# Performance work log

Measured on AMD Instinct MI355X. Metric: run time of the kernel, lower is better.

Reference implementation:

```python
import jax, jax.numpy as jnp
import numpy as np

TOP_K = 2


def setup_inputs() -> dict:
    key = jax.random.key(0)
    k1, k2, k3, k4, k5 = jax.random.split(key, 5)
    H, F, E = 1024, 2048, 8
    B, S = 2, 1024
    return {
        "hidden_states": jax.random.normal(k1, (B, S, H), dtype=jnp.float32),
        "gate_w": jax.random.normal(k2, (E, H), dtype=jnp.float32) * (1.0 / np.sqrt(H)),
        "w1": jax.random.normal(k3, (E, F, H), dtype=jnp.float32) * (1.0 / np.sqrt(H)),
        "w2": jax.random.normal(k4, (E, H, F), dtype=jnp.float32) * (1.0 / np.sqrt(F)),
        "w3": jax.random.normal(k5, (E, F, H), dtype=jnp.float32) * (1.0 / np.sqrt(H)),
    }


def reference(hidden_states, gate_w, w1, w2, w3):
    B, S, H = hidden_states.shape
    E = gate_w.shape[0]
    x = hidden_states.reshape(-1, H)  # [T, H]

    # Router: softmax in float32, top-k, renormalize (exact Mixtral math)
    router_logits = x @ gate_w.T  # [T, E]
    probs = jax.nn.softmax(router_logits.astype(jnp.float32), axis=-1)
    routing_weights, selected = jax.lax.top_k(probs, TOP_K)  # [T, K]
    routing_weights = routing_weights / routing_weights.sum(axis=-1, keepdims=True)
    routing_weights = routing_weights.astype(x.dtype)

    # Per-token combine weight for each expert: [T, E]
    combine = (jax.nn.one_hot(selected, E, dtype=x.dtype) * routing_weights[..., None]).sum(axis=1)

    # Dense grouped expert SwiGLU MLP (zero combine weight for unselected experts
    # makes this strictly equivalent to the gathered/dispatched computation)
    h = jnp.einsum('th,efh->etf', x, w1)   # [E, T, F]
    g = jnp.einsum('th,efh->etf', x, w3)   # [E, T, F]
    mid = jax.nn.silu(h) * g               # SwiGLU
    expert_out = jnp.einsum('etf,ehf->eth', mid, w2)  # [E, T, H]
    out = jnp.einsum('eth,te->th', expert_out, combine)  # weighted combine

    return out.reshape(B, S, H), router_logits
```

## Files before the change

### kernel.cpp

```cpp
#include <hip/hip_runtime.h>
#include <hip/hip_bf16.h>
#include <math.h>

#define H 1024
#define FF 2048
#define E 8
#define T 2048
#define NSLOT (2*T)
#define SLOT_PAD 128

typedef __attribute__((ext_vector_type(8))) short s16x8;
typedef __attribute__((ext_vector_type(4))) float f32x4;

static __device__ __forceinline__ unsigned short f2bf(float f) {
    union { float f; unsigned u; } v; v.f = f;
    unsigned r = v.u + 0x7fff + ((v.u >> 16) & 1);
    return (unsigned short)(r >> 16);
}
static __device__ __forceinline__ float bf2f(unsigned short s) {
    union { unsigned u; float f; } v; v.u = ((unsigned)s) << 16;
    return v.f;
}

typedef __attribute__((address_space(3))) unsigned int lds_uint;
typedef const __attribute__((address_space(1))) unsigned int glob_uint;
static __device__ __forceinline__ void gl_lds16(const void* g, void* l) {
    __builtin_amdgcn_global_load_lds((glob_uint*)g, (lds_uint*)l, 16, 0, 0);
}

__global__ __launch_bounds__(256) void convert_kernel(
    const float* __restrict__ w1, const float* __restrict__ w3,
    const float* __restrict__ w2, unsigned short* __restrict__ w1b,
    unsigned short* __restrict__ w3b, unsigned short* __restrict__ w2b)
{
    const float* s; unsigned short* d;
    if (blockIdx.y == 0)      { s = w1; d = w1b; }
    else if (blockIdx.y == 1) { s = w3; d = w3b; }
    else                      { s = w2; d = w2b; }
    size_t i = ((size_t)blockIdx.x * 256 + threadIdx.x) * 8;
    float4 a = *(const float4*)(s + i);
    float4 b = *(const float4*)(s + i + 4);
    uint4 st;
    st.x = f2bf(a.x) | ((unsigned)f2bf(a.y) << 16);
    st.y = f2bf(a.z) | ((unsigned)f2bf(a.w) << 16);
    st.z = f2bf(b.x) | ((unsigned)f2bf(b.y) << 16);
    st.w = f2bf(b.z) | ((unsigned)f2bf(b.w) << 16);
    *(uint4*)(d + i) = st;
}

__global__ __launch_bounds__(256) void router_kernel(
    const float* __restrict__ x, const float* __restrict__ gw,
    float* __restrict__ logits_out, int* __restrict__ top_id,
    float* __restrict__ top_w, int* __restrict__ counts)
{
    int t = blockIdx.x;
    int tid = threadIdx.x;
    int e = tid >> 5;
    int l32 = tid & 31;
    const float* xr = x + (size_t)t * H;
    const float* gr = gw + (size_t)e * H;
    float s = 0.f;
    for (int h = l32; h < H; h += 32) s += xr[h] * gr[h];
    for (int off = 16; off; off >>= 1) s += __shfl_down(s, off, 32);
    __shared__ float lg[E];
    if (l32 == 0) lg[e] = s;
    __syncthreads();
    if (tid < E) logits_out[(size_t)t * E + tid] = lg[tid];
    if (tid == 0) {
        int i1 = 0; float b1 = lg[0];
        for (int i = 1; i < E; ++i) if (lg[i] > b1) { b1 = lg[i]; i1 = i; }
        int i2 = -1; float b2 = -INFINITY;
        for (int i = 0; i < E; ++i) if (i != i1 && lg[i] > b2) { b2 = lg[i]; i2 = i; }
        float p2 = expf(b2 - b1);
        float inv = 1.f / (1.f + p2);
        top_id[2*t]   = i1;  top_id[2*t+1] = i2;
        top_w[2*t]    = inv; top_w[2*t+1]  = p2 * inv;
        atomicAdd(&counts[i1], 1);
        atomicAdd(&counts[i2], 1);
    }
}

__global__ void scan_kernel(const int* __restrict__ counts,
                            int* __restrict__ offsets, int* __restrict__ cursors)
{
    if (threadIdx.x == 0) {
        int acc = 0;
        for (int i = 0; i < E; ++i) { offsets[i] = acc; acc += counts[i]; }
        offsets[E] = acc;
    }
    if (threadIdx.x < E) cursors[threadIdx.x] = 0;
}

__global__ __launch_bounds__(256) void assign_kernel(
    const float* __restrict__ x, const int* __restrict__ top_id,
    const int* __restrict__ offsets, int* __restrict__ cursors,
    int* __restrict__ top_pos, unsigned short* __restrict__ xg)
{
    int t = blockIdx.x, tid = threadIdx.x;
    __shared__ int pos[2];
    if (tid == 0) {
        for (int k = 0; k < 2; ++k) {
            int e = top_id[2*t + k];
            int p = offsets[e] + atomicAdd(&cursors[e], 1);
            top_pos[2*t + k] = p;
            pos[k] = p;
        }
    }
    __syncthreads();
    float4 xv = ((const float4*)(x + (size_t)t * H))[tid];
    ushort4 b;
    b.x = f2bf(xv.x); b.y = f2bf(xv.y); b.z = f2bf(xv.z); b.w = f2bf(xv.w);
    ((ushort4*)(xg + (size_t)pos[0] * H))[tid] = b;
    ((ushort4*)(xg + (size_t)pos[1] * H))[tid] = b;
}

__global__ __launch_bounds__(256) void gemm1_kernel(
    const unsigned short* __restrict__ xg,
    const unsigned short* __restrict__ w1b, const unsigned short* __restrict__ w3b,
    const int* __restrict__ offsets, unsigned short* __restrict__ mid)
{
    int e = blockIdx.z;
    int off = offsets[e];
    int cnt = offsets[e + 1] - off;
    int m0 = blockIdx.y * 128;
    if (m0 >= cnt) return;
    int f0 = blockIdx.x * 64;

    __shared__ __align__(16) unsigned short sx[128 * 64];
    __shared__ __align__(16) unsigned short s1[64 * 64];
    __shared__ __align__(16) unsigned short s3[64 * 64];

    int tid = threadIdx.x;
    int wv = tid >> 6, ln = tid & 63;
    int quad = ln >> 4, l16 = ln & 15;
    int wm = wv & 1, wn = wv >> 1;
    int xor7 = l16 & 7;

    const unsigned short* xsrc[4]; unsigned short* xdst[4];
    #pragma unroll
    for (int j = 0; j < 4; ++j) {
        int row = wv * 32 + j * 8 + (ln >> 3);
        int cl = (ln & 7) ^ (row & 7);
        xsrc[j] = xg + (size_t)(off + m0 + row) * H + cl * 8;
        xdst[j] = &sx[(wv * 32 + j * 8) * 64];
    }
    const unsigned short *w1s[2], *w3s[2]; unsigned short *d1[2], *d3[2];
    #pragma unroll
    for (int j = 0; j < 2; ++j) {
        int row = wv * 16 + j * 8 + (ln >> 3);
        int cl = (ln & 7) ^ (row & 7);
        w1s[j] = w1b + ((size_t)e * FF + f0 + row) * H + cl * 8;
        w3s[j] = w3b + ((size_t)e * FF + f0 + row) * H + cl * 8;
        d1[j] = &s1[(wv * 16 + j * 8) * 64];
        d3[j] = &s3[(wv * 16 + j * 8) * 64];
    }

    f32x4 acc1[4][2], acc3[4][2];
    #pragma unroll
    for (int i = 0; i < 4; ++i)
        #pragma unroll
        for (int j = 0; j < 2; ++j) {
            acc1[i][j] = (f32x4){0.f, 0.f, 0.f, 0.f};
            acc3[i][j] = (f32x4){0.f, 0.f, 0.f, 0.f};
        }

    for (int k0 = 0; k0 < H; k0 += 64) {
        #pragma unroll
        for (int j = 0; j < 4; ++j) gl_lds16(xsrc[j] + k0, xdst[j]);
        #pragma unroll
        for (int j = 0; j < 2; ++j) { gl_lds16(w1s[j] + k0, d1[j]); gl_lds16(w3s[j] + k0, d3[j]); }
        __syncthreads();
        #pragma unroll
        for (int ks = 0; ks < 2; ++ks) {
            int cph = ((quad + 4 * ks) ^ xor7) << 3;
            s16x8 a[4], b1v[2], b3v[2];
            #pragma unroll
            for (int i = 0; i < 4; ++i)
                a[i] = *(const s16x8*)&sx[(wm * 64 + i * 16 + l16) * 64 + cph];
            #pragma unroll
            for (int j = 0; j < 2; ++j) {
                b1v[j] = *(const s16x8*)&s1[(wn * 32 + j * 16 + l16) * 64 + cph];
                b3v[j] = *(const s16x8*)&s3[(wn * 32 + j * 16 + l16) * 64 + cph];
            }
            #pragma unroll
            for (int i = 0; i < 4; ++i)
                #pragma unroll
                for (int j = 0; j < 2; ++j) {
                    acc1[i][j] = __builtin_amdgcn_mfma_f32_16x16x32_bf16(a[i], b1v[j], acc1[i][j], 0, 0, 0);
                    acc3[i][j] = __builtin_amdgcn_mfma_f32_16x16x32_bf16(a[i], b3v[j], acc3[i][j], 0, 0, 0);
                }
        }
        __syncthreads();
    }

    #pragma unroll
    for (int i = 0; i < 4; ++i) {
        #pragma unroll
        for (int r = 0; r < 4; ++r) {
            int row = wm * 64 + i * 16 + quad * 4 + r;
            if (m0 + row < cnt) {
                size_t base = (size_t)(off + m0 + row) * FF + f0 + wn * 32;
                #pragma unroll
                for (int j = 0; j < 2; ++j) {
                    float h = acc1[i][j][r];
                    float g = acc3[i][j][r];
                    float v = h / (1.f + __expf(-h)) * g;
                    mid[base + j * 16 + l16] = f2bf(v);
                }
            }
        }
    }
}

__global__ __launch_bounds__(256) void gemm2_kernel(
    const unsigned short* __restrict__ mid, const unsigned short* __restrict__ w2b,
    const int* __restrict__ offsets, unsigned short* __restrict__ y)
{
    int e = blockIdx.z;
    int off = offsets[e];
    int cnt = offsets[e + 1] - off;
    int m0 = blockIdx.y * 128;
    if (m0 >= cnt) return;
    int n0 = blockIdx.x * 64;

    __shared__ __align__(16) unsigned short sa[128 * 64];
    __shared__ __align__(16) unsigned short sb[64 * 64];

    int tid = threadIdx.x;
    int wv = tid >> 6, ln = tid & 63;
    int quad = ln >> 4, l16 = ln & 15;
    int wm = wv & 1, wn = wv >> 1;
    int xor7 = l16 & 7;

    const unsigned short* asrc[4]; unsigned short* adst[4];
    #pragma unroll
    for (int j = 0; j < 4; ++j) {
        int row = wv * 32 + j * 8 + (ln >> 3);
        int cl = (ln & 7) ^ (row & 7);
        asrc[j] = mid + (size_t)(off + m0 + row) * FF + cl * 8;
        adst[j] = &sa[(wv * 32 + j * 8) * 64];
    }
    const unsigned short* bsrc[2]; unsigned short* bdst[2];
    #pragma unroll
    for (int j = 0; j < 2; ++j) {
        int row = wv * 16 + j * 8 + (ln >> 3);
        int cl = (ln & 7) ^ (row & 7);
        bsrc[j] = w2b + ((size_t)e * H + n0 + row) * FF + cl * 8;
        bdst[j] = &sb[(wv * 16 + j * 8) * 64];
    }

    f32x4 acc[4][2];
    #pragma unroll
    for (int i = 0; i < 4; ++i)
        #pragma unroll
        for (int j = 0; j < 2; ++j) acc[i][j] = (f32x4){0.f, 0.f, 0.f, 0.f};

    for (int k0 = 0; k0 < FF; k0 += 64) {
        #pragma unroll
        for (int j = 0; j < 4; ++j) gl_lds16(asrc[j] + k0, adst[j]);
        #pragma unroll
        for (int j = 0; j < 2; ++j) gl_lds16(bsrc[j] + k0, bdst[j]);
        __syncthreads();
        #pragma unroll
        for (int ks = 0; ks < 2; ++ks) {
            int cph = ((quad + 4 * ks) ^ xor7) << 3;
            s16x8 a[4], b[2];
            #pragma unroll
            for (int i = 0; i < 4; ++i)
                a[i] = *(const s16x8*)&sa[(wm * 64 + i * 16 + l16) * 64 + cph];
            #pragma unroll
            for (int j = 0; j < 2; ++j)
                b[j] = *(const s16x8*)&sb[(wn * 32 + j * 16 + l16) * 64 + cph];
            #pragma unroll
            for (int i = 0; i < 4; ++i)
                #pragma unroll
                for (int j = 0; j < 2; ++j)
                    acc[i][j] = __builtin_amdgcn_mfma_f32_16x16x32_bf16(a[i], b[j], acc[i][j], 0, 0, 0);
        }
        __syncthreads();
    }

    #pragma unroll
    for (int i = 0; i < 4; ++i) {
        #pragma unroll
        for (int r = 0; r < 4; ++r) {
            int row = wm * 64 + i * 16 + quad * 4 + r;
            if (m0 + row < cnt) {
                size_t base = (size_t)(off + m0 + row) * H + n0 + wn * 32;
                #pragma unroll
                for (int j = 0; j < 2; ++j)
                    y[base + j * 16 + l16] = f2bf(acc[i][j][r]);
            }
        }
    }
}

__global__ __launch_bounds__(256) void combine_kernel(
    const unsigned short* __restrict__ y, const int* __restrict__ top_pos,
    const float* __restrict__ top_w, float* __restrict__ out)
{
    int t = blockIdx.x, tid = threadIdx.x;
    int p0 = top_pos[2*t], p1 = top_pos[2*t+1];
    float w0 = top_w[2*t], w1 = top_w[2*t+1];
    ushort4 a = ((const ushort4*)(y + (size_t)p0 * H))[tid];
    ushort4 b = ((const ushort4*)(y + (size_t)p1 * H))[tid];
    float4 o;
    o.x = w0 * bf2f(a.x) + w1 * bf2f(b.x);
    o.y = w0 * bf2f(a.y) + w1 * bf2f(b.y);
    o.z = w0 * bf2f(a.z) + w1 * bf2f(b.z);
    o.w = w0 * bf2f(a.w) + w1 * bf2f(b.w);
    ((float4*)(out + (size_t)t * H))[tid] = o;
}

extern "C" void kernel_launch(void* const* d_in, const int* in_sizes, int n_in,
                              void* d_out, int out_size, void* d_ws, size_t ws_size,
                              hipStream_t stream) {
    const float* x  = (const float*)d_in[0];
    const float* gw = (const float*)d_in[1];
    const float* w1 = (const float*)d_in[2];
    const float* w2 = (const float*)d_in[3];
    const float* w3 = (const float*)d_in[4];
    float* out    = (float*)d_out;
    float* logits = out + (size_t)T * H;

    int* counts   = (int*)d_ws;
    int* cursors  = counts + 8;
    int* offsets  = counts + 16;
    int* top_id   = counts + 32;
    int* top_pos  = top_id + 2*T;
    float* top_w  = (float*)(top_pos + 2*T);
    unsigned short* xg  = (unsigned short*)(top_w + 2*T);
    unsigned short* mid = xg  + (size_t)(NSLOT + SLOT_PAD) * H;
    unsigned short* y   = mid + (size_t)(NSLOT + SLOT_PAD) * FF;
    unsigned short* w1b = y   + (size_t)NSLOT * H;
    unsigned short* w3b = w1b + (size_t)E * FF * H;
    unsigned short* w2b = w3b + (size_t)E * FF * H;

    hipMemsetAsync(counts, 0, 16 * sizeof(int), stream);

    convert_kernel<<<dim3((E*FF*H)/(256*8), 3), 256, 0, stream>>>(w1, w3, w2, w1b, w3b, w2b);
    router_kernel<<<T, 256, 0, stream>>>(x, gw, logits, top_id, top_w, counts);
    scan_kernel<<<1, 64, 0, stream>>>(counts, offsets, cursors);
    assign_kernel<<<T, 256, 0, stream>>>(x, top_id, offsets, cursors, top_pos, xg);
    gemm1_kernel<<<dim3(FF / 64, 16, E), 256, 0, stream>>>(xg, w1b, w3b, offsets, mid);
    gemm2_kernel<<<dim3(H / 64, 16, E), 256, 0, stream>>>(mid, w2b, offsets, y);
    combine_kernel<<<T, 256, 0, stream>>>(y, top_pos, top_w, out);
}
```

Before: 426.3 us.

## Fuse weight conversion with router, drop scan, gather tokens via slot index in GEMM1

Merges weight conversion, x conversion and routing into one prep kernel. The scan kernel is removed: offsets are recomputed from counts inside each kernel. The per-slot copy of bf16 x is replaced by a slot-to-token table that GEMM1 uses to gather rows directly. Conversion now moves 16 elements per thread with nontemporal loads. Together these cut launches and the duplicated xg write traffic, at the cost of an indirect row gather in GEMM1.

```diff
diff --git a/kernel.cpp b/kernel.cpp
--- a/kernel.cpp
+++ b/kernel.cpp
@@ -9,8 +9,14 @@
 #define NSLOT (2*T)
 #define SLOT_PAD 128
 
+#define WCONV_BLKS 12288
+#define XCONV_BLKS 512
+#define ROUTER_BLKS T
+#define K1_BLKS (WCONV_BLKS + XCONV_BLKS + ROUTER_BLKS)
+
 typedef __attribute__((ext_vector_type(8))) short s16x8;
 typedef __attribute__((ext_vector_type(4))) float f32x4;
+typedef __attribute__((ext_vector_type(4))) unsigned int u32x4;
 
 static __device__ __forceinline__ unsigned short f2bf(float f) {
     union { float f; unsigned u; } v; v.f = f;
@@ -21,6 +27,9 @@
     union { unsigned u; float f; } v; v.u = ((unsigned)s) << 16;
     return v.f;
 }
+static __device__ __forceinline__ unsigned pack2(float a, float b) {
+    return (unsigned)f2bf(a) | ((unsigned)f2bf(b) << 16);
+}
 
 typedef __attribute__((address_space(3))) unsigned int lds_uint;
 typedef const __attribute__((address_space(1))) unsigned int glob_uint;
@@ -28,33 +37,54 @@
     __builtin_amdgcn_global_load_lds((glob_uint*)g, (lds_uint*)l, 16, 0, 0);
 }
 
-__global__ __launch_bounds__(256) void convert_kernel(
+static __device__ __forceinline__ void expert_range(const int* __restrict__ counts,
+                                                    int e, int& off, int& cnt) {
+    int acc = 0;
+    #pragma unroll
+    for (int i = 0; i < E; ++i) {
+        int c = counts[i];
+        if (i < e) acc += c;
+        if (i == e) cnt = c;
+    }
+    off = acc;
+}
+
+__global__ __launch_bounds__(256) void prep_kernel(
+    const float* __restrict__ x, const float* __restrict__ gw,
     const float* __restrict__ w1, const float* __restrict__ w3,
-    const float* __restrict__ w2, unsigned short* __restrict__ w1b,
-    unsigned short* __restrict__ w3b, unsigned short* __restrict__ w2b)
-{
-    const float* s; unsigned short* d;
-    if (blockIdx.y == 0)      { s = w1; d = w1b; }
-    else if (blockIdx.y == 1) { s = w3; d = w3b; }
-    else                      { s = w2; d = w2b; }
-    size_t i = ((size_t)blockIdx.x * 256 + threadIdx.x) * 8;
-    float4 a = *(const float4*)(s + i);
-    float4 b = *(const float4*)(s + i + 4);
-    uint4 st;
-    st.x = f2bf(a.x) | ((unsigned)f2bf(a.y) << 16);
-    st.y = f2bf(a.z) | ((unsigned)f2bf(a.w) << 16);
-    st.z = f2bf(b.x) | ((unsigned)f2bf(b.y) << 16);
-    st.w = f2bf(b.z) | ((unsigned)f2bf(b.w) << 16);
-    *(uint4*)(d + i) = st;
-}
-
-__global__ __launch_bounds__(256) void router_kernel(
-    const float* __restrict__ x, const float* __restrict__ gw,
+    const float* __restrict__ w2,
+    unsigned short* __restrict__ w1b, unsigned short* __restrict__ w3b,
+    unsigned short* __restrict__ w2b, unsigned short* __restrict__ xb,
     float* __restrict__ logits_out, int* __restrict__ top_id,
     float* __restrict__ top_w, int* __restrict__ counts)
 {
-    int t = blockIdx.x;
+    int b = blockIdx.x;
     int tid = threadIdx.x;
+    if (b < WCONV_BLKS + XCONV_BLKS) {
+        const float* s; unsigned short* d; size_t i;
+        if (b < WCONV_BLKS) {
+            int r = b >> 12;
+            s = (r == 0) ? w1 : (r == 1) ? w3 : w2;
+            d = (r == 0) ? w1b : (r == 1) ? w3b : w2b;
+            i = ((size_t)(b & 4095) * 256 + tid) * 16;
+        } else {
+            s = x; d = xb;
+            i = ((size_t)(b - WCONV_BLKS) * 256 + tid) * 16;
+        }
+        f32x4 a0 = __builtin_nontemporal_load((const f32x4*)(s + i));
+        f32x4 a1 = __builtin_nontemporal_load((const f32x4*)(s + i + 4));
+        f32x4 a2 = __builtin_nontemporal_load((const f32x4*)(s + i + 8));
+        f32x4 a3 = __builtin_nontemporal_load((const f32x4*)(s + i + 12));
+        u32x4 r0, r1;
+        r0.x = pack2(a0.x, a0.y); r0.y = pack2(a0.z, a0.w);
+        r0.z = pack2(a1.x, a1.y); r0.w = pack2(a1.z, a1.w);
+        r1.x = pack2(a2.x, a2.y); r1.y = pack2(a2.z, a2.w);
+        r1.z = pack2(a3.x, a3.y); r1.w = pack2(a3.z, a3.w);
+        *(u32x4*)(d + i) = r0;
+        *(u32x4*)(d + i + 8) = r1;
+        return;
+    }
+    int t = b - (WCONV_BLKS + XCONV_BLKS);
     int e = tid >> 5;
     int l32 = tid & 31;
     const float* xr = x + (size_t)t * H;
@@ -80,48 +110,36 @@
     }
 }
 
-__global__ void scan_kernel(const int* __restrict__ counts,
-                            int* __restrict__ offsets, int* __restrict__ cursors)
-{
-    if (threadIdx.x == 0) {
+__global__ __launch_bounds__(256) void assign_kernel(
+    const int* __restrict__ top_id, const int* __restrict__ counts,
+    int* __restrict__ cursors, int* __restrict__ top_pos,
+    int* __restrict__ slot_token)
+{
+    int t = blockIdx.x * 256 + threadIdx.x;
+    if (t >= T) return;
+    int offs[E];
+    {
         int acc = 0;
-        for (int i = 0; i < E; ++i) { offsets[i] = acc; acc += counts[i]; }
-        offsets[E] = acc;
-    }
-    if (threadIdx.x < E) cursors[threadIdx.x] = 0;
-}
-
-__global__ __launch_bounds__(256) void assign_kernel(
-    const float* __restrict__ x, const int* __restrict__ top_id,
-    const int* __restrict__ offsets, int* __restrict__ cursors,
-    int* __restrict__ top_pos, unsigned short* __restrict__ xg)
-{
-    int t = blockIdx.x, tid = threadIdx.x;
-    __shared__ int pos[2];
-    if (tid == 0) {
-        for (int k = 0; k < 2; ++k) {
-            int e = top_id[2*t + k];
-            int p = offsets[e] + atomicAdd(&cursors[e], 1);
-            top_pos[2*t + k] = p;
-            pos[k] = p;
-        }
-    }
-    __syncthreads();
-    float4 xv = ((const float4*)(x + (size_t)t * H))[tid];
-    ushort4 b;
-    b.x = f2bf(xv.x); b.y = f2bf(xv.y); b.z = f2bf(xv.z); b.w = f2bf(xv.w);
-    ((ushort4*)(xg + (size_t)pos[0] * H))[tid] = b;
-    ((ushort4*)(xg + (size_t)pos[1] * H))[tid] = b;
+        #pragma unroll
+        for (int i = 0; i < E; ++i) { offs[i] = acc; acc += counts[i]; }
+    }
+    #pragma unroll
+    for (int k = 0; k < 2; ++k) {
+        int e = top_id[2*t + k];
+        int p = offs[e] + atomicAdd(&cursors[e], 1);
+        top_pos[2*t + k] = p;
+        slot_token[p] = t;
+    }
 }
 
 __global__ __launch_bounds__(256) void gemm1_kernel(
-    const unsigned short* __restrict__ xg,
+    const unsigned short* __restrict__ xb, const int* __restrict__ slot_token,
     const unsigned short* __restrict__ w1b, const unsigned short* __restrict__ w3b,
-    const int* __restrict__ offsets, unsigned short* __restrict__ mid)
+    const int* __restrict__ counts, unsigned short* __restrict__ mid)
 {
     int e = blockIdx.z;
-    int off = offsets[e];
-    int cnt = offsets[e + 1] - off;
+    int off, cnt;
+    expert_range(counts, e, off, cnt);
     int m0 = blockIdx.y * 128;
     if (m0 >= cnt) return;
     int f0 = blockIdx.x * 64;
@@ -140,8 +158,11 @@
     #pragma unroll
     for (int j = 0; j < 4; ++j) {
         int row = wv * 32 + j * 8 + (ln >> 3);
+        int slot = off + m0 + row;
+        if (m0 + row >= cnt) slot = off;
+        int tok = slot_token[slot];
         int cl = (ln & 7) ^ (row & 7);
-        xsrc[j] = xg + (size_t)(off + m0 + row) * H + cl * 8;
+        xsrc[j] = xb + (size_t)tok * H + cl * 8;
         xdst[j] = &sx[(wv * 32 + j * 8) * 64];
     }
     const unsigned short *w1s[2], *w3s[2]; unsigned short *d1[2], *d3[2];
@@ -214,11 +235,11 @@
 
 __global__ __launch_bounds__(256) void gemm2_kernel(
     const unsigned short* __restrict__ mid, const unsigned short* __restrict__ w2b,
-    const int* __restrict__ offsets, unsigned short* __restrict__ y)
+    const int* __restrict__ counts, unsigned short* __restrict__ y)
 {
     int e = blockIdx.z;
-    int off = offsets[e];
-    int cnt = offsets[e + 1] - off;
+    int off, cnt;
+    expert_range(counts, e, off, cnt);
     int m0 = blockIdx.y * 128;
     if (m0 >= cnt) return;
     int n0 = blockIdx.x * 64;
@@ -323,26 +344,28 @@
     float* out    = (float*)d_out;
     float* logits = out + (size_t)T * H;
 
-    int* counts   = (int*)d_ws;
-    int* cursors  = counts + 8;
-    int* offsets  = counts + 16;
-    int* top_id   = counts + 32;
-    int* top_pos  = top_id + 2*T;
-    float* top_w  = (float*)(top_pos + 2*T);
-    unsigned short* xg  = (unsigned short*)(top_w + 2*T);
-    unsigned short* mid = xg  + (size_t)(NSLOT + SLOT_PAD) * H;
+    int* counts      = (int*)d_ws;
+    int* cursors     = counts + 8;
+    int* top_id      = counts + 16;
+    int* top_pos     = top_id + 2*T;
+    int* slot_token  = top_pos + 2*T;
+    float* top_w     = (float*)(slot_token + NSLOT);
+    unsigned short* xb  = (unsigned short*)(top_w + 2*T);
+    unsigned short* mid = xb  + (size_t)T * H;
     unsigned short* y   = mid + (size_t)(NSLOT + SLOT_PAD) * FF;
     unsigned short* w1b = y   + (size_t)NSLOT * H;
     unsigned short* w3b = w1b + (size_t)E * FF * H;
     unsigned short* w2b = w3b + (size_t)E * FF * H;
 
-    hipMemsetAsync(counts, 0, 16 * sizeof(int), stream);
-
-    convert_kernel<<<dim3((E*FF*H)/(256*8), 3), 256, 0, stream>>>(w1, w3, w2, w1b, w3b, w2b);
-    router_kernel<<<T, 256, 0, stream>>>(x, gw, logits, top_id, top_w, counts);
-    scan_kernel<<<1, 64, 0, stream>>>(counts, offsets, cursors);
-    assign_kernel<<<T, 256, 0, stream>>>(x, top_id, offsets, cursors, top_pos, xg);
-    gemm1_kernel<<<dim3(FF / 64, 16, E), 256, 0, stream>>>(xg, w1b, w3b, offsets, mid);
-    gemm2_kernel<<<dim3(H / 64, 16, E), 256, 0, stream>>>(mid, w2b, offsets, y);
+    (void)hipMemsetAsync(counts, 0, 16 * sizeof(int), stream);
+
+    prep_kernel<<<K1_BLKS, 256, 0, stream>>>(x, gw, w1, w3, w2,
+                                             w1b, w3b, w2b, xb,
+                                             logits, top_id, top_w, counts);
+    assign_kernel<<<(T + 255) / 256, 256, 0, stream>>>(top_id, counts, cursors,
+                                                       top_pos, slot_token);
+    gemm1_kernel<<<dim3(FF / 64, 16, E), 256, 0, stream>>>(xb, slot_token,
+                                                           w1b, w3b, counts, mid);
+    gemm2_kernel<<<dim3(H / 64, 16, E), 256, 0, stream>>>(mid, w2b, counts, y);
     combine_kernel<<<T, 256, 0, stream>>>(y, top_pos, top_w, out);
 }
```

Result: no change. 422.9 us (-0.8%).
